# Kernel tuning notes

Measured on AMD Instinct MI355X. Metric: run time of the kernel, lower is better.

Reference implementation:

```python
import jax, jax.numpy as jnp
import numpy as np

B, D, H, O, S, K, T = 4096, 512, 1024, 512, 4, 4, 3


def setup_inputs() -> dict:
    key = jax.random.key(0)
    ks = iter(jax.random.split(key, 48))
    def w(*shape):
        return jax.random.normal(next(ks), shape, jnp.float32) * 0.02
    def z(*shape):
        return jnp.zeros(shape, jnp.float32)
    return {
        'user_emb': jax.random.normal(next(ks), (B, D), jnp.float32),
        # layer-1 shared experts (stacked over S): D -> H -> O
        's1_W1': w(S, D, H), 's1_b1': z(S, H), 's1_W2': w(S, H, O), 's1_b2': z(S, O),
        # layer-1 task experts (stacked over T tasks x K experts)
        't1_W1': w(T, K, D, H), 't1_b1': z(T, K, H), 't1_W2': w(T, K, H, O), 't1_b2': z(T, K, O),
        # layer-1 gates: T task gates (S+K outputs) + 1 combined gate (S+T*K outputs)
        'g1_W': w(T, D, S + K), 'g1_b': z(T, S + K),
        'g1l_W': w(D, S + T * K), 'g1l_b': z(S + T * K),
        # layer-2 shared / task experts: O -> H -> O
        's2_W1': w(S, O, H), 's2_b1': z(S, H), 's2_W2': w(S, H, O), 's2_b2': z(S, O),
        't2_W1': w(T, K, O, H), 't2_b1': z(T, K, H), 't2_W2': w(T, K, H, O), 't2_b2': z(T, K, O),
        'g2_W': w(T, O, S + K), 'g2_b': z(T, S + K),
        # churn tower: O -> 512 -> 256 -> 1
        'ch_W1': w(O, 512), 'ch_b1': z(512), 'ch_W2': w(512, 256), 'ch_b2': z(256), 'ch_W3': w(256, 1), 'ch_b3': z(1),
        # buy_sku + buy_cat towers stacked on leading axis 2: O -> 512 -> 256 -> 100
        'bt_W1': w(2, O, 512), 'bt_b1': z(2, 512), 'bt_W2': w(2, 512, 256), 'bt_b2': z(2, 256), 'bt_W3': w(2, 256, 100), 'bt_b3': z(2, 100),
    }


def _ple_forward(user_emb, s1_W1, s1_b1, s1_W2, s1_b2, t1_W1, t1_b1, t1_W2, t1_b2,
                 g1_W, g1_b, g1l_W, g1l_b, s2_W1, s2_b1, s2_W2, s2_b2,
                 t2_W1, t2_b1, t2_W2, t2_b2, g2_W, g2_b,
                 ch_W1, ch_b1, ch_W2, ch_b2, ch_W3, ch_b3,
                 bt_W1, bt_b1, bt_W2, bt_b2, bt_W3, bt_b3):
    relu = jax.nn.relu
    Bn = user_emb.shape[0]
    # ---- PLE layer 1 (dropout = identity in eval) ----
    sh1 = jnp.einsum('bsh,sho->bso', relu(jnp.einsum('bd,sdh->bsh', user_emb, s1_W1) + s1_b1), s1_W2) + s1_b2          # [B,S,O]
    tk1 = jnp.einsum('btkh,tkho->btko', relu(jnp.einsum('bd,tkdh->btkh', user_emb, t1_W1) + t1_b1), t1_W2) + t1_b2    # [B,T,K,O]
    g1 = jax.nn.softmax(jnp.einsum('bd,tde->tbe', user_emb, g1_W) + g1_b[:, None, :], axis=-1)                        # [T,B,S+K]
    g1l = jax.nn.softmax(user_emb @ g1l_W + g1l_b, axis=-1)                                                           # [B,S+T*K]
    # per-task concat: [shared, task_i] experts, gated combine (bmm)
    feats = jnp.concatenate([jnp.broadcast_to(sh1[:, None], (Bn, T, S, O)), tk1], axis=2)                             # [B,T,S+K,O]
    task_feats = jnp.einsum('tbe,bteo->tbo', g1, feats)                                                               # [T,B,O]
    # combined feat: order is [task_0..task_{T-1}, shared] per the torch code
    feats_last = jnp.concatenate([tk1.reshape(Bn, T * K, O), sh1], axis=1)                                            # [B,T*K+S,O]
    feat_last = jnp.einsum('be,beo->bo', g1l, feats_last)                                                             # [B,O]
    # ---- PLE layer 2 ----
    sh2 = jnp.einsum('bsh,sho->bso', relu(jnp.einsum('bo,soh->bsh', feat_last, s2_W1) + s2_b1), s2_W2) + s2_b2        # [B,S,O]
    tk2 = jnp.einsum('tbkh,tkho->tbko', relu(jnp.einsum('tbo,tkoh->tbkh', task_feats, t2_W1) + t2_b1[:, None]), t2_W2) + t2_b2[:, None]  # [T,B,K,O]
    g2 = jax.nn.softmax(jnp.einsum('tbo,toe->tbe', task_feats, g2_W) + g2_b[:, None, :], axis=-1)                     # [T,B,S+K]
    exp2 = jnp.concatenate([jnp.broadcast_to(sh2[None], (T, Bn, S, O)), tk2], axis=2)                                 # [T,B,S+K,O]
    tower_in = jnp.einsum('tbe,tbeo->tbo', g2, exp2)                                                                  # [T,B,O]
    # ---- towers ----
    churn = relu(relu(tower_in[0] @ ch_W1 + ch_b1) @ ch_W2 + ch_b2) @ ch_W3 + ch_b3                                   # [B,1]
    x = tower_in[1:3]                                                                                                 # [2,B,O]
    h = relu(jnp.einsum('nbo,noh->nbh', x, bt_W1) + bt_b1[:, None])
    h = relu(jnp.einsum('nbh,nhk->nbk', h, bt_W2) + bt_b2[:, None])
    out = jnp.einsum('nbk,nkm->nbm', h, bt_W3) + bt_b3[:, None]                                                       # [2,B,100]
    return churn, out[0], out[1]


def reference(user_emb, s1_W1, s1_b1, s1_W2, s1_b2, t1_W1, t1_b1, t1_W2, t1_b2,
              g1_W, g1_b, g1l_W, g1l_b, s2_W1, s2_b1, s2_W2, s2_b2,
              t2_W1, t2_b1, t2_W2, t2_b2, g2_W, g2_b,
              ch_W1, ch_b1, ch_W2, ch_b2, ch_W3, ch_b3,
              bt_W1, bt_b1, bt_W2, bt_b2, bt_W3, bt_b3):
    return _ple_forward(user_emb, s1_W1, s1_b1, s1_W2, s1_b2, t1_W1, t1_b1, t1_W2, t1_b2,
                        g1_W, g1_b, g1l_W, g1l_b, s2_W1, s2_b1, s2_W2, s2_b2,
                        t2_W1, t2_b1, t2_W2, t2_b2, g2_W, g2_b,
                        ch_W1, ch_b1, ch_W2, ch_b2, ch_W3, ch_b3,
                        bt_W1, bt_b1, bt_W2, bt_b2, bt_W3, bt_b3)
```

## Files before the change

kernel.cpp:

```cpp
#include <hip/hip_runtime.h>
#include <stdint.h>
#include <stddef.h>

typedef float f32x4 __attribute__((ext_vector_type(4)));
typedef int   i32x4 __attribute__((ext_vector_type(4)));
typedef _Float16 f16;
typedef _Float16 f16x8 __attribute__((ext_vector_type(8)));
typedef _Float16 f16x4 __attribute__((ext_vector_type(4)));

#define NB 4096

__device__ __forceinline__ size_t tiled_off(int m, int k, int K) {
  return (size_t)(m >> 7) * ((size_t)128 * K) + (size_t)(k >> 5) * 4096 +
         (size_t)(((k >> 3) & 3) * 1024 + (m & 127) * 8 + (k & 7));
}

__device__ __forceinline__ void gload_lds16(const f16* g, f16* l) {
  __builtin_amdgcn_global_load_lds(
      (const __attribute__((address_space(1))) void*)g,
      (__attribute__((address_space(3))) void*)l, 16, 0, 0);
}

struct GemmArgs {
  const f16* A[16];
  const f16* W[16];
  const float* bias[16];
  void* C[16];
  int N, K;
};

template<bool RELU, int OMODE>
__global__ __launch_bounds__(256, 4)
void gemm_kernel(GemmArgs args) {
  const int nwg = gridDim.x * gridDim.y * gridDim.z;
  int bid = blockIdx.x + gridDim.x * (blockIdx.y + gridDim.y * blockIdx.z);
  if ((nwg & 7) == 0) {
    const int cpx = nwg >> 3;
    bid = (bid & 7) * cpx + (bid >> 3);
  }
  const int gx  = bid % gridDim.x;
  const int rem = bid / gridDim.x;
  const int gy  = rem % gridDim.y;
  const int g   = rem / gridDim.y;
  const int n0 = gx * 128, m0 = gy * 128;

  const int tid = threadIdx.x;
  const int lane = tid & 63;
  const int wid = tid >> 6;
  const int wr = wid >> 1, wc = wid & 1;
  const int N = args.N, K = args.K;

  __shared__ __align__(16) f16 SH[16384];

  const f16* __restrict__ At = args.A[g] + (size_t)gy * 128 * K;
  const f16* __restrict__ Wt = args.W[g] + (size_t)gx * 128 * K;

  const int e0 = tid * 8, e1 = e0 + 2048;
  const int wb0 = (tid & ~63) * 8;
  const int wb1 = wb0 + 2048;

  f32x4 acc[4][4];
#pragma unroll
  for (int i = 0; i < 4; i++)
#pragma unroll
    for (int j = 0; j < 4; j++) { f32x4 z = {0.f, 0.f, 0.f, 0.f}; acc[i][j] = z; }

  const int nsteps = K >> 5;

  {
    f16* ab = SH;
    f16* bb = SH + 8192;
    gload_lds16(At + e0, ab + wb0);
    gload_lds16(At + e1, ab + wb1);
    gload_lds16(Wt + e0, bb + wb0);
    gload_lds16(Wt + e1, bb + wb1);
  }
  __syncthreads();

  for (int s = 0; s < nsteps; ++s) {
    const int cur = s & 1;
    if (s + 1 < nsteps) {
      const int nxt = cur ^ 1;
      const int off = (s + 1) << 12;
      f16* ab = SH + nxt * 4096;
      f16* bb = SH + 8192 + nxt * 4096;
      gload_lds16(At + off + e0, ab + wb0);
      gload_lds16(At + off + e1, ab + wb1);
      gload_lds16(Wt + off + e0, bb + wb0);
      gload_lds16(Wt + off + e1, bb + wb1);
    }
    const f16* ab = SH + cur * 4096;
    const f16* bb = SH + 8192 + cur * 4096;
    f16x8 af[4], bfv[4];
#pragma unroll
    for (int i = 0; i < 4; i++)
      af[i] = *(const f16x8*)(ab + (lane >> 4) * 1024 + (wr * 64 + i * 16 + (lane & 15)) * 8);
#pragma unroll
    for (int j = 0; j < 4; j++)
      bfv[j] = *(const f16x8*)(bb + (lane >> 4) * 1024 + (wc * 64 + j * 16 + (lane & 15)) * 8);
#pragma unroll
    for (int i = 0; i < 4; i++)
#pragma unroll
      for (int j = 0; j < 4; j++)
        acc[i][j] = __builtin_amdgcn_mfma_f32_16x16x32_f16(af[i], bfv[j], acc[i][j], 0, 0, 0);
    if (s + 1 < nsteps) __syncthreads();
  }

  const float* __restrict__ bias = args.bias[g];

  if constexpr (OMODE == 2) {
    __syncthreads();
#pragma unroll
    for (int j = 0; j < 4; j++) {
      const int col = wc * 64 + j * 16 + (lane & 15);
      const float bv = bias[n0 + col];
#pragma unroll
      for (int i = 0; i < 4; i++) {
        const int rowb = wr * 64 + i * 16 + ((lane >> 4) << 2);
#pragma unroll
        for (int q = 0; q < 4; q++) {
          float v = acc[i][j][q] + bv;
          if (RELU) v = fmaxf(v, 0.0f);
          SH[tiled_off(rowb + q, col, 128)] = (f16)v;
        }
      }
    }
    __syncthreads();
    f16* __restrict__ Cg = (f16*)args.C[g] + ((size_t)gy * N + n0) * 128;
#pragma unroll
    for (int r = 0; r < 8; r++) {
      const int c = r * 256 + tid;
      i32x4 v = *(const i32x4*)(SH + (size_t)c * 8);
      *(i32x4*)(Cg + (size_t)c * 8) = v;
    }
  } else {
#pragma unroll
    for (int j = 0; j < 4; j++) {
      const int n = n0 + wc * 64 + j * 16 + (lane & 15);
      if (n < N) {
        const float bv = bias[n];
#pragma unroll
        for (int i = 0; i < 4; i++) {
          const int mrow = m0 + wr * 64 + i * 16 + ((lane >> 4) << 2);
#pragma unroll
          for (int q = 0; q < 4; q++) {
            float v = acc[i][j][q] + bv;
            if (RELU) v = fmaxf(v, 0.0f);
            ((float*)args.C[g])[(size_t)(mrow + q) * N + n] = v;
          }
        }
      }
    }
  }
}

__global__ __launch_bounds__(256)
void transpose_cvt2_kernel(const float* __restrict__ srcA, int nA,
                           const float* __restrict__ srcB,
                           f16* __restrict__ dst, int K, int N, int dstStride) {
  __shared__ float tile[32][33];
  const int z = blockIdx.z;
  const float* __restrict__ src =
      (z < nA) ? srcA + (size_t)z * K * N : srcB + (size_t)(z - nA) * K * N;
  const size_t dof = (size_t)z * dstStride;
  const int kb = blockIdx.y * 32, nb = blockIdx.x * 32;
  const int tx = threadIdx.x, ty = threadIdx.y;
#pragma unroll
  for (int i = 0; i < 32; i += 8) {
    int k = kb + ty + i, n = nb + tx;
    tile[ty + i][tx] = (k < K && n < N) ? src[(size_t)k * N + n] : 0.f;
  }
  __syncthreads();
#pragma unroll
  for (int i = 0; i < 32; i += 8) {
    int n = nb + ty + i, k = kb + tx;
    if (n < N && k < K) dst[dof + tiled_off(n, k, K)] = (f16)tile[tx][ty + i];
  }
}

__global__ __launch_bounds__(256)
void cvt_kernel(const float* __restrict__ src, f16* __restrict__ dst, int n4) {
  int i = blockIdx.x * 256 + threadIdx.x;
  if (i < n4) {
    f32x4 v = *(const f32x4*)(src + (size_t)i * 4);
    f16x4 o = {(f16)v.x, (f16)v.y, (f16)v.z, (f16)v.w};
    const int e = i * 4;
    *(f16x4*)(dst + tiled_off(e >> 9, e & 511, 512)) = o;
  }
}

__global__ __launch_bounds__(256)
void gates1_kernel(const float* __restrict__ x, const float* __restrict__ g1W,
                   const float* __restrict__ g1b, const float* __restrict__ g1lW,
                   const float* __restrict__ g1lb, float* __restrict__ g1,
                   float* __restrict__ g1l) {
  const int lane = threadIdx.x & 63;
  const int b = blockIdx.x * 4 + (threadIdx.x >> 6);
  float xv[8];
#pragma unroll
  for (int i = 0; i < 8; i++) xv[i] = x[(size_t)b * 512 + lane + 64 * i];

#pragma unroll
  for (int t = 0; t < 3; t++) {
    float acc[8] = {0, 0, 0, 0, 0, 0, 0, 0};
#pragma unroll
    for (int i = 0; i < 8; i++) {
      const int d = lane + 64 * i;
      const float* wp = g1W + ((size_t)t * 512 + d) * 8;
      f32x4 w0 = *(const f32x4*)wp;
      f32x4 w1 = *(const f32x4*)(wp + 4);
      acc[0] += xv[i] * w0.x; acc[1] += xv[i] * w0.y;
      acc[2] += xv[i] * w0.z; acc[3] += xv[i] * w0.w;
      acc[4] += xv[i] * w1.x; acc[5] += xv[i] * w1.y;
      acc[6] += xv[i] * w1.z; acc[7] += xv[i] * w1.w;
    }
#pragma unroll
    for (int e = 0; e < 8; e++) {
#pragma unroll
      for (int off = 32; off >= 1; off >>= 1) acc[e] += __shfl_xor(acc[e], off);
      acc[e] += g1b[t * 8 + e];
    }
    float m = acc[0];
#pragma unroll
    for (int e = 1; e < 8; e++) m = fmaxf(m, acc[e]);
    float s = 0.f, p[8];
#pragma unroll
    for (int e = 0; e < 8; e++) { p[e] = expf(acc[e] - m); s += p[e]; }
    float inv = 1.0f / s;
    float mine = 0.f;
#pragma unroll
    for (int e = 0; e < 8; e++) if (lane == e) mine = p[e] * inv;
    if (lane < 8) g1[((size_t)t * NB + b) * 8 + lane] = mine;
  }

  float acc[16] = {};
#pragma unroll
  for (int i = 0; i < 8; i++) {
    const int d = lane + 64 * i;
    const float* wp = g1lW + (size_t)d * 16;
#pragma unroll
    for (int e4 = 0; e4 < 4; e4++) {
      f32x4 wv = *(const f32x4*)(wp + e4 * 4);
      acc[e4 * 4 + 0] += xv[i] * wv.x; acc[e4 * 4 + 1] += xv[i] * wv.y;
      acc[e4 * 4 + 2] += xv[i] * wv.z; acc[e4 * 4 + 3] += xv[i] * wv.w;
    }
  }
#pragma unroll
  for (int e = 0; e < 16; e++) {
#pragma unroll
    for (int off = 32; off >= 1; off >>= 1) acc[e] += __shfl_xor(acc[e], off);
    acc[e] += g1lb[e];
  }
  float m = acc[0];
#pragma unroll
  for (int e = 1; e < 16; e++) m = fmaxf(m, acc[e]);
  float s = 0.f, p[16];
#pragma unroll
  for (int e = 0; e < 16; e++) { p[e] = expf(acc[e] - m); s += p[e]; }
  float inv = 1.0f / s;
  float mine = 0.f;
#pragma unroll
  for (int e = 0; e < 16; e++) if (lane == e) mine = p[e] * inv;
  if (lane < 16) g1l[(size_t)b * 16 + lane] = mine;
}

__global__ __launch_bounds__(256)
void gates2_kernel(const f16* __restrict__ tf, const float* __restrict__ g2W,
                   const float* __restrict__ g2b, float* __restrict__ g2, int Bc) {
  const int lane = threadIdx.x & 63;
  const int b = blockIdx.x * 4 + (threadIdx.x >> 6);
  const int t = blockIdx.y;
  const f16* tb = tf + (size_t)t * Bc * 512;
  float xv[8];
#pragma unroll
  for (int i = 0; i < 8; i++)
    xv[i] = (float)tb[tiled_off(b, lane + 64 * i, 512)];
  float acc[8] = {0, 0, 0, 0, 0, 0, 0, 0};
#pragma unroll
  for (int i = 0; i < 8; i++) {
    const int d = lane + 64 * i;
    const float* wp = g2W + ((size_t)t * 512 + d) * 8;
    f32x4 w0 = *(const f32x4*)wp;
    f32x4 w1 = *(const f32x4*)(wp + 4);
    acc[0] += xv[i] * w0.x; acc[1] += xv[i] * w0.y;
    acc[2] += xv[i] * w0.z; acc[3] += xv[i] * w0.w;
    acc[4] += xv[i] * w1.x; acc[5] += xv[i] * w1.y;
    acc[6] += xv[i] * w1.z; acc[7] += xv[i] * w1.w;
  }
#pragma unroll
  for (int e = 0; e < 8; e++) {
#pragma unroll
    for (int off = 32; off >= 1; off >>= 1) acc[e] += __shfl_xor(acc[e], off);
    acc[e] += g2b[t * 8 + e];
  }
  float m = acc[0];
#pragma unroll
  for (int e = 1; e < 8; e++) m = fmaxf(m, acc[e]);
  float s = 0.f, p[8];
#pragma unroll
  for (int e = 0; e < 8; e++) { p[e] = expf(acc[e] - m); s += p[e]; }
  float inv = 1.0f / s;
  float mine = 0.f;
#pragma unroll
  for (int e = 0; e < 8; e++) if (lane == e) mine = p[e] * inv;
  if (lane < 8) g2[((size_t)t * Bc + b) * 8 + lane] = mine;
}

__global__ __launch_bounds__(256)
void combine1_kernel(const f16* __restrict__ E, const float* __restrict__ g1,
                     const float* __restrict__ g1l, f16* __restrict__ tfh,
                     f16* __restrict__ flh, int Bc) {
  const int t8 = blockIdx.x * 256 + threadIdx.x;
  const int b = ((t8 >> 13) << 7) | (t8 & 127);
  const size_t base = (size_t)t8 * 8;
  f16x8 ev[16];
#pragma unroll
  for (int i = 0; i < 16; i++)
    ev[i] = *(const f16x8*)(E + (size_t)i * Bc * 512 + base);
#pragma unroll
  for (int t = 0; t < 3; t++) {
    const float* g = g1 + ((size_t)t * NB + b) * 8;
    f16x8 o;
#pragma unroll
    for (int j = 0; j < 8; j++) {
      float v = g[0] * (float)ev[0][j] + g[1] * (float)ev[1][j] +
                g[2] * (float)ev[2][j] + g[3] * (float)ev[3][j];
#pragma unroll
      for (int k = 0; k < 4; k++) v += g[4 + k] * (float)ev[4 + 4 * t + k][j];
      o[j] = (f16)v;
    }
    *(f16x8*)(tfh + (size_t)t * Bc * 512 + base) = o;
  }
  const float* gl = g1l + (size_t)b * 16;
  f16x8 o;
#pragma unroll
  for (int j = 0; j < 8; j++) {
    float v = 0.f;
#pragma unroll
    for (int jj = 0; jj < 12; jj++) v += gl[jj] * (float)ev[4 + jj][j];
#pragma unroll
    for (int s2 = 0; s2 < 4; s2++) v += gl[12 + s2] * (float)ev[s2][j];
    o[j] = (f16)v;
  }
  *(f16x8*)(flh + base) = o;
}

__global__ __launch_bounds__(256)
void combine2_kernel(const f16* __restrict__ E2, const float* __restrict__ g2,
                     f16* __restrict__ tin, int Bc) {
  const int t = blockIdx.y;
  const int t8 = blockIdx.x * 256 + threadIdx.x;
  const int b = ((t8 >> 13) << 7) | (t8 & 127);
  const size_t base = (size_t)t8 * 8;
  const float* g = g2 + ((size_t)t * Bc + b) * 8;
  f16x8 es[8];
#pragma unroll
  for (int s2 = 0; s2 < 4; s2++)
    es[s2] = *(const f16x8*)(E2 + (size_t)s2 * Bc * 512 + base);
#pragma unroll
  for (int k = 0; k < 4; k++)
    es[4 + k] = *(const f16x8*)(E2 + (size_t)(4 + 4 * t + k) * Bc * 512 + base);
  f16x8 o;
#pragma unroll
  for (int j = 0; j < 8; j++) {
    float v = 0.f;
#pragma unroll
    for (int i = 0; i < 8; i++) v += g[i] * (float)es[i][j];
    o[j] = (f16)v;
  }
  *(f16x8*)(tin + (size_t)t * Bc * 512 + base) = o;
}

__global__ __launch_bounds__(256)
void churn_l3_kernel(const f16* __restrict__ TW2, const float* __restrict__ W3,
                     const float* __restrict__ b3, float* __restrict__ out) {
  const int lane = threadIdx.x & 63;
  const int b = blockIdx.x * 4 + (threadIdx.x >> 6);
  float s = 0.f;
#pragma unroll
  for (int i = 0; i < 4; i++) {
    int d = lane + 64 * i;
    s += (float)TW2[tiled_off(b, d, 256)] * W3[d];
  }
#pragma unroll
  for (int off = 32; off >= 1; off >>= 1) s += __shfl_xor(s, off);
  if (lane == 0) out[b] = s + b3[0];
}

extern "C" void kernel_launch(void* const* d_in, const int* in_sizes, int n_in,
                              void* d_out, int out_size, void* d_ws, size_t ws_size,
                              hipStream_t stream) {
  const float* user_emb = (const float*)d_in[0];
  const float* s1_W1 = (const float*)d_in[1];
  const float* s1_b1 = (const float*)d_in[2];
  const float* s1_W2 = (const float*)d_in[3];
  const float* s1_b2 = (const float*)d_in[4];
  const float* t1_W1 = (const float*)d_in[5];
  const float* t1_b1 = (const float*)d_in[6];
  const float* t1_W2 = (const float*)d_in[7];
  const float* t1_b2 = (const float*)d_in[8];
  const float* g1_W  = (const float*)d_in[9];
  const float* g1_b  = (const float*)d_in[10];
  const float* g1l_W = (const float*)d_in[11];
  const float* g1l_b = (const float*)d_in[12];
  const float* s2_W1 = (const float*)d_in[13];
  const float* s2_b1 = (const float*)d_in[14];
  const float* s2_W2 = (const float*)d_in[15];
  const float* s2_b2 = (const float*)d_in[16];
  const float* t2_W1 = (const float*)d_in[17];
  const float* t2_b1 = (const float*)d_in[18];
  const float* t2_W2 = (const float*)d_in[19];
  const float* t2_b2 = (const float*)d_in[20];
  const float* g2_W  = (const float*)d_in[21];
  const float* g2_b  = (const float*)d_in[22];
  const float* ch_W1 = (const float*)d_in[23];
  const float* ch_b1 = (const float*)d_in[24];
  const float* ch_W2 = (const float*)d_in[25];
  const float* ch_b2 = (const float*)d_in[26];
  const float* ch_W3 = (const float*)d_in[27];
  const float* ch_b3 = (const float*)d_in[28];
  const float* bt_W1 = (const float*)d_in[29];
  const float* bt_b1 = (const float*)d_in[30];
  const float* bt_W2 = (const float*)d_in[31];
  const float* bt_b2 = (const float*)d_in[32];
  const float* bt_W3 = (const float*)d_in[33];
  const float* bt_b3 = (const float*)d_in[34];

  const size_t PERSIST = 74800000ull;
  const size_t PERCHUNK_PER_ROW = 61024ull;
  int Bc = 4096;
  while (Bc > 256 &&
         PERSIST + PERCHUNK_PER_ROW * (size_t)Bc + (64ull << 10) > ws_size)
    Bc >>= 1;
  const int nchunks = NB / Bc;

  char* w = (char*)d_ws;
  auto alloc = [&](size_t bytes) {
    char* p = w;
    w += (bytes + 255) & ~(size_t)255;
    return p;
  };
  f16* WT1 = (f16*)alloc(16ull * 512 * 1024 * 2);
  f16* WT2 = (f16*)alloc(16ull * 1024 * 512 * 2);
  f16* WT3 = (f16*)alloc(16ull * 512 * 1024 * 2);
  f16* WT4 = (f16*)alloc(16ull * 1024 * 512 * 2);
  f16* WT5 = (f16*)alloc(3ull * 512 * 512 * 2);
  f16* WT6 = (f16*)alloc(3ull * 256 * 512 * 2);
  f16* WT7 = (f16*)alloc(2ull * 128 * 256 * 2);
  f16* Uemb = (f16*)alloc((size_t)NB * 512 * 2);
  float* B1  = (float*)alloc(16384 * 4);
  float* B2  = (float*)alloc(8192 * 4);
  float* B3  = (float*)alloc(16384 * 4);
  float* B4  = (float*)alloc(8192 * 4);
  float* BT1 = (float*)alloc(1536 * 4);
  float* BT2 = (float*)alloc(768 * 4);
  float* G1  = (float*)alloc(3ull * NB * 8 * 4);
  float* G1L = (float*)alloc((size_t)NB * 16 * 4);
  f16*   Hc   = (f16*)alloc(16ull * Bc * 1024 * 2);
  f16*   Ec   = (f16*)alloc(16ull * Bc * 512 * 2);
  f16*   TFh  = (f16*)alloc(3ull * Bc * 512 * 2);
  f16*   FLh  = (f16*)alloc((size_t)Bc * 512 * 2);
  float* G2c  = (float*)alloc(3ull * Bc * 8 * 4);
  f16*   TINc = (f16*)alloc(3ull * Bc * 512 * 2);
  f16*   TW1c = (f16*)alloc(3ull * Bc * 512 * 2);
  f16*   TW2c = (f16*)alloc(3ull * Bc * 256 * 2);
  if ((size_t)(w - (char*)d_ws) > ws_size) return;

  hipMemcpyAsync(B1, s1_b1, 4 * 1024 * 4, hipMemcpyDeviceToDevice, stream);
  hipMemcpyAsync(B1 + 4096, t1_b1, 12 * 1024 * 4, hipMemcpyDeviceToDevice, stream);
  hipMemcpyAsync(B2, s1_b2, 4 * 512 * 4, hipMemcpyDeviceToDevice, stream);
  hipMemcpyAsync(B2 + 2048, t1_b2, 12 * 512 * 4, hipMemcpyDeviceToDevice, stream);
  hipMemcpyAsync(B3, s2_b1, 4 * 1024 * 4, hipMemcpyDeviceToDevice, stream);
  hipMemcpyAsync(B3 + 4096, t2_b1, 12 * 1024 * 4, hipMemcpyDeviceToDevice, stream);
  hipMemcpyAsync(B4, s2_b2, 4 * 512 * 4, hipMemcpyDeviceToDevice, stream);
  hipMemcpyAsync(B4 + 2048, t2_b2, 12 * 512 * 4, hipMemcpyDeviceToDevice, stream);
  hipMemcpyAsync(BT1, ch_b1, 512 * 4, hipMemcpyDeviceToDevice, stream);
  hipMemcpyAsync(BT1 + 512, bt_b1, 2 * 512 * 4, hipMemcpyDeviceToDevice, stream);
  hipMemcpyAsync(BT2, ch_b2, 256 * 4, hipMemcpyDeviceToDevice, stream);
  hipMemcpyAsync(BT2 + 256, bt_b2, 2 * 256 * 4, hipMemcpyDeviceToDevice, stream);
  hipMemsetAsync(WT7, 0, 2ull * 128 * 256 * 2, stream);

  dim3 tb(32, 8);
  transpose_cvt2_kernel<<<dim3(32, 16, 16), tb, 0, stream>>>(s1_W1, 4, t1_W1, WT1, 512, 1024, 512 * 1024);
  transpose_cvt2_kernel<<<dim3(16, 32, 16), tb, 0, stream>>>(s1_W2, 4, t1_W2, WT2, 1024, 512, 1024 * 512);
  transpose_cvt2_kernel<<<dim3(32, 16, 16), tb, 0, stream>>>(s2_W1, 4, t2_W1, WT3, 512, 1024, 512 * 1024);
  transpose_cvt2_kernel<<<dim3(16, 32, 16), tb, 0, stream>>>(s2_W2, 4, t2_W2, WT4, 1024, 512, 1024 * 512);
  transpose_cvt2_kernel<<<dim3(16, 16, 3), tb, 0, stream>>>(ch_W1, 1, bt_W1, WT5, 512, 512, 512 * 512);
  transpose_cvt2_kernel<<<dim3(8, 16, 3), tb, 0, stream>>>(ch_W2, 1, bt_W2, WT6, 512, 256, 256 * 512);
  transpose_cvt2_kernel<<<dim3(4, 8, 2), tb, 0, stream>>>(bt_W3, 2, nullptr, WT7, 256, 100, 128 * 256);
  cvt_kernel<<<2048, 256, 0, stream>>>(user_emb, Uemb, NB * 512 / 4);
  gates1_kernel<<<NB / 4, 256, 0, stream>>>(user_emb, g1_W, g1_b, g1l_W, g1l_b, G1, G1L);

  GemmArgs ga;
  const int MB = Bc / 128;

  for (int c = 0; c < nchunks; ++c) {
    const int b0 = c * Bc;

    ga.N = 1024; ga.K = 512;
    for (int g = 0; g < 16; g++) {
      ga.A[g] = Uemb + (size_t)b0 * 512;
      ga.W[g] = WT1 + (size_t)g * 512 * 1024;
      ga.bias[g] = B1 + g * 1024;
      ga.C[g] = Hc + (size_t)g * Bc * 1024;
    }
    gemm_kernel<true, 2><<<dim3(8, MB, 16), 256, 0, stream>>>(ga);

    ga.N = 512; ga.K = 1024;
    for (int g = 0; g < 16; g++) {
      ga.A[g] = Hc + (size_t)g * Bc * 1024;
      ga.W[g] = WT2 + (size_t)g * 1024 * 512;
      ga.bias[g] = B2 + g * 512;
      ga.C[g] = Ec + (size_t)g * Bc * 512;
    }
    gemm_kernel<false, 2><<<dim3(4, MB, 16), 256, 0, stream>>>(ga);

    combine1_kernel<<<Bc / 4, 256, 0, stream>>>(
        Ec, G1 + (size_t)b0 * 8, G1L + (size_t)b0 * 16, TFh, FLh, Bc);
    gates2_kernel<<<dim3(Bc / 4, 3), 256, 0, stream>>>(TFh, g2_W, g2_b, G2c, Bc);

    ga.N = 1024; ga.K = 512;
    for (int g = 0; g < 16; g++) {
      ga.A[g] = (g < 4) ? FLh : TFh + (size_t)((g - 4) >> 2) * Bc * 512;
      ga.W[g] = WT3 + (size_t)g * 512 * 1024;
      ga.bias[g] = B3 + g * 1024;
      ga.C[g] = Hc + (size_t)g * Bc * 1024;
    }
    gemm_kernel<true, 2><<<dim3(8, MB, 16), 256, 0, stream>>>(ga);

    ga.N = 512; ga.K = 1024;
    for (int g = 0; g < 16; g++) {
      ga.A[g] = Hc + (size_t)g * Bc * 1024;
      ga.W[g] = WT4 + (size_t)g * 1024 * 512;
      ga.bias[g] = B4 + g * 512;
      ga.C[g] = Ec + (size_t)g * Bc * 512;
    }
    gemm_kernel<false, 2><<<dim3(4, MB, 16), 256, 0, stream>>>(ga);

    combine2_kernel<<<dim3(Bc / 4, 3), 256, 0, stream>>>(Ec, G2c, TINc, Bc);

    ga.N = 512; ga.K = 512;
    for (int g = 0; g < 3; g++) {
      ga.A[g] = TINc + (size_t)g * Bc * 512;
      ga.W[g] = WT5 + (size_t)g * 512 * 512;
      ga.bias[g] = BT1 + g * 512;
      ga.C[g] = TW1c + (size_t)g * Bc * 512;
    }
    for (int g = 3; g < 16; g++) { ga.A[g] = ga.A[0]; ga.W[g] = ga.W[0]; ga.bias[g] = ga.bias[0]; ga.C[g] = ga.C[0]; }
    gemm_kernel<true, 2><<<dim3(4, MB, 3), 256, 0, stream>>>(ga);

    ga.N = 256; ga.K = 512;
    for (int g = 0; g < 3; g++) {
      ga.A[g] = TW1c + (size_t)g * Bc * 512;
      ga.W[g] = WT6 + (size_t)g * 256 * 512;
      ga.bias[g] = BT2 + g * 256;
      ga.C[g] = TW2c + (size_t)g * Bc * 256;
    }
    for (int g = 3; g < 16; g++) { ga.A[g] = ga.A[0]; ga.W[g] = ga.W[0]; ga.bias[g] = ga.bias[0]; ga.C[g] = ga.C[0]; }
    gemm_kernel<true, 2><<<dim3(2, MB, 3), 256, 0, stream>>>(ga);

    churn_l3_kernel<<<Bc / 4, 256, 0, stream>>>(TW2c, ch_W3, ch_b3,
                                                (float*)d_out + b0);

    ga.N = 100; ga.K = 256;
    for (int g = 0; g < 2; g++) {
      ga.A[g] = TW2c + (size_t)(1 + g) * Bc * 256;
      ga.W[g] = WT7 + (size_t)g * 128 * 256;
      ga.bias[g] = bt_b3 + g * 100;
      ga.C[g] = (float*)d_out + NB + (size_t)g * NB * 100 + (size_t)b0 * 100;
    }
    for (int g = 2; g < 16; g++) { ga.A[g] = ga.A[0]; ga.W[g] = ga.W[0]; ga.bias[g] = ga.bias[0]; ga.C[g] = ga.C[0]; }
    gemm_kernel<false, 0><<<dim3(1, MB, 2), 256, 0, stream>>>(ga);
  }
}
```

Baseline: 545.9 us.

## Vectorize weight transpose, fuse bias packing into one kernel, swizzle GEMM epilogue LDS

Rewrites the weight transpose/convert kernel to use 64x64 tiles with float4 global loads and 16-byte f16x8 stores. Replaces twelve device-to-device bias memcpys and a memset with a single packing kernel, cutting per-call launch overhead. Adds an XOR swizzle to the GEMM f16 epilogue's shared-memory staging to reduce bank conflicts. The transpose relies on K being a multiple of 64 and uses a larger shared tile, which may lower occupancy.

Result: faster. 504.4 us (-7.6%).

```diff
diff --git a/kernel.cpp b/kernel.cpp
--- a/kernel.cpp
+++ b/kernel.cpp
@@ -110,6 +110,7 @@
 
   if constexpr (OMODE == 2) {
     __syncthreads();
+    const int swz = (((lane >> 3) & 1) << 3) | (((lane >> 5) & 1) << 4);
 #pragma unroll
     for (int j = 0; j < 4; j++) {
       const int col = wc * 64 + j * 16 + (lane & 15);
@@ -121,7 +122,7 @@
         for (int q = 0; q < 4; q++) {
           float v = acc[i][j][q] + bv;
           if (RELU) v = fmaxf(v, 0.0f);
-          SH[tiled_off(rowb + q, col, 128)] = (f16)v;
+          SH[tiled_off(rowb + q, col, 128) ^ swz] = (f16)v;
         }
       }
     }
@@ -130,7 +131,8 @@
 #pragma unroll
     for (int r = 0; r < 8; r++) {
       const int c = r * 256 + tid;
-      i32x4 v = *(const i32x4*)(SH + (size_t)c * 8);
+      const int te = (c * 8) ^ (((c >> 7) & 1) << 3) ^ (((c >> 3) & 1) << 4);
+      i32x4 v = *(const i32x4*)(SH + te);
       *(i32x4*)(Cg + (size_t)c * 8) = v;
     }
   } else {
@@ -158,23 +160,42 @@
 void transpose_cvt2_kernel(const float* __restrict__ srcA, int nA,
                            const float* __restrict__ srcB,
                            f16* __restrict__ dst, int K, int N, int dstStride) {
-  __shared__ float tile[32][33];
+  __shared__ float tile[64][67];
   const int z = blockIdx.z;
   const float* __restrict__ src =
       (z < nA) ? srcA + (size_t)z * K * N : srcB + (size_t)(z - nA) * K * N;
   const size_t dof = (size_t)z * dstStride;
-  const int kb = blockIdx.y * 32, nb = blockIdx.x * 32;
-  const int tx = threadIdx.x, ty = threadIdx.y;
-#pragma unroll
-  for (int i = 0; i < 32; i += 8) {
-    int k = kb + ty + i, n = nb + tx;
-    tile[ty + i][tx] = (k < K && n < N) ? src[(size_t)k * N + n] : 0.f;
+  const int nb = blockIdx.x * 64, kb = blockIdx.y * 64;
+  const int tid = threadIdx.x;
+  const int krow = tid >> 4;
+  const int n4 = (tid & 15) * 4;
+#pragma unroll
+  for (int i = 0; i < 4; i++) {
+    const int kk = krow + i * 16;
+    const int k = kb + kk;
+    const int n = nb + n4;
+    if (n + 3 < N) {
+      f32x4 v = *(const f32x4*)(src + (size_t)k * N + n);
+      tile[kk][n4 + 0] = v.x; tile[kk][n4 + 1] = v.y;
+      tile[kk][n4 + 2] = v.z; tile[kk][n4 + 3] = v.w;
+    } else {
+#pragma unroll
+      for (int e = 0; e < 4; e++)
+        tile[kk][n4 + e] = (n + e < N) ? src[(size_t)k * N + n + e] : 0.f;
+    }
   }
   __syncthreads();
-#pragma unroll
-  for (int i = 0; i < 32; i += 8) {
-    int n = nb + ty + i, k = kb + tx;
-    if (n < N && k < K) dst[dof + tiled_off(n, k, K)] = (f16)tile[tx][ty + i];
+  const int o = tid >> 5;
+  const int nl = tid & 31;
+#pragma unroll
+  for (int j = 0; j < 2; j++) {
+    const int n = nl + j * 32;
+    if (nb + n < N) {
+      f16x8 v;
+#pragma unroll
+      for (int e = 0; e < 8; e++) v[e] = (f16)tile[o * 8 + e][n];
+      *(f16x8*)(dst + dof + tiled_off(nb + n, kb + o * 8, K)) = v;
+    }
   }
 }
 
@@ -187,6 +208,30 @@
     const int e = i * 4;
     *(f16x4*)(dst + tiled_off(e >> 9, e & 511, 512)) = o;
   }
+}
+
+__global__ __launch_bounds__(256)
+void pack_kernel(float* B1, const float* s1b1, const float* t1b1,
+                 float* B2, const float* s1b2, const float* t1b2,
+                 float* B3, const float* s2b1, const float* t2b1,
+                 float* B4, const float* s2b2, const float* t2b2,
+                 float* BT1, const float* chb1, const float* btb1,
+                 float* BT2, const float* chb2, const float* btb2,
+                 uint32_t* wt7z) {
+  int i = blockIdx.x * 256 + threadIdx.x;
+  if (i < 16384) { B1[i] = (i < 4096) ? s1b1[i] : t1b1[i - 4096]; return; }
+  i -= 16384;
+  if (i < 8192)  { B2[i] = (i < 2048) ? s1b2[i] : t1b2[i - 2048]; return; }
+  i -= 8192;
+  if (i < 16384) { B3[i] = (i < 4096) ? s2b1[i] : t2b1[i - 4096]; return; }
+  i -= 16384;
+  if (i < 8192)  { B4[i] = (i < 2048) ? s2b2[i] : t2b2[i - 2048]; return; }
+  i -= 8192;
+  if (i < 1536)  { BT1[i] = (i < 512) ? chb1[i] : btb1[i - 512]; return; }
+  i -= 1536;
+  if (i < 768)   { BT2[i] = (i < 256) ? chb2[i] : btb2[i - 256]; return; }
+  i -= 768;
+  if (i < 32768) wt7z[i] = 0u;
 }
 
 __global__ __launch_bounds__(256)
@@ -466,28 +511,18 @@
   f16*   TW2c = (f16*)alloc(3ull * Bc * 256 * 2);
   if ((size_t)(w - (char*)d_ws) > ws_size) return;
 
-  hipMemcpyAsync(B1, s1_b1, 4 * 1024 * 4, hipMemcpyDeviceToDevice, stream);
-  hipMemcpyAsync(B1 + 4096, t1_b1, 12 * 1024 * 4, hipMemcpyDeviceToDevice, stream);
-  hipMemcpyAsync(B2, s1_b2, 4 * 512 * 4, hipMemcpyDeviceToDevice, stream);
-  hipMemcpyAsync(B2 + 2048, t1_b2, 12 * 512 * 4, hipMemcpyDeviceToDevice, stream);
-  hipMemcpyAsync(B3, s2_b1, 4 * 1024 * 4, hipMemcpyDeviceToDevice, stream);
-  hipMemcpyAsync(B3 + 4096, t2_b1, 12 * 1024 * 4, hipMemcpyDeviceToDevice, stream);
-  hipMemcpyAsync(B4, s2_b2, 4 * 512 * 4, hipMemcpyDeviceToDevice, stream);
-  hipMemcpyAsync(B4 + 2048, t2_b2, 12 * 512 * 4, hipMemcpyDeviceToDevice, stream);
-  hipMemcpyAsync(BT1, ch_b1, 512 * 4, hipMemcpyDeviceToDevice, stream);
-  hipMemcpyAsync(BT1 + 512, bt_b1, 2 * 512 * 4, hipMemcpyDeviceToDevice, stream);
-  hipMemcpyAsync(BT2, ch_b2, 256 * 4, hipMemcpyDeviceToDevice, stream);
-  hipMemcpyAsync(BT2 + 256, bt_b2, 2 * 256 * 4, hipMemcpyDeviceToDevice, stream);
-  hipMemsetAsync(WT7, 0, 2ull * 128 * 256 * 2, stream);
-
-  dim3 tb(32, 8);
-  transpose_cvt2_kernel<<<dim3(32, 16, 16), tb, 0, stream>>>(s1_W1, 4, t1_W1, WT1, 512, 1024, 512 * 1024);
-  transpose_cvt2_kernel<<<dim3(16, 32, 16), tb, 0, stream>>>(s1_W2, 4, t1_W2, WT2, 1024, 512, 1024 * 512);
-  transpose_cvt2_kernel<<<dim3(32, 16, 16), tb, 0, stream>>>(s2_W1, 4, t2_W1, WT3, 512, 1024, 512 * 1024);
-  transpose_cvt2_kernel<<<dim3(16, 32, 16), tb, 0, stream>>>(s2_W2, 4, t2_W2, WT4, 1024, 512, 1024 * 512);
-  transpose_cvt2_kernel<<<dim3(16, 16, 3), tb, 0, stream>>>(ch_W1, 1, bt_W1, WT5, 512, 512, 512 * 512);
-  transpose_cvt2_kernel<<<dim3(8, 16, 3), tb, 0, stream>>>(ch_W2, 1, bt_W2, WT6, 512, 256, 256 * 512);
-  transpose_cvt2_kernel<<<dim3(4, 8, 2), tb, 0, stream>>>(bt_W3, 2, nullptr, WT7, 256, 100, 128 * 256);
+  pack_kernel<<<329, 256, 0, stream>>>(B1, s1_b1, t1_b1, B2, s1_b2, t1_b2,
+                                       B3, s2_b1, t2_b1, B4, s2_b2, t2_b2,
+                                       BT1, ch_b1, bt_b1, BT2, ch_b2, bt_b2,
+                                       (uint32_t*)WT7);
+
+  transpose_cvt2_kernel<<<dim3(16, 8, 16), 256, 0, stream>>>(s1_W1, 4, t1_W1, WT1, 512, 1024, 512 * 1024);
+  transpose_cvt2_kernel<<<dim3(8, 16, 16), 256, 0, stream>>>(s1_W2, 4, t1_W2, WT2, 1024, 512, 1024 * 512);
+  transpose_cvt2_kernel<<<dim3(16, 8, 16), 256, 0, stream>>>(s2_W1, 4, t2_W1, WT3, 512, 1024, 512 * 1024);
+  transpose_cvt2_kernel<<<dim3(8, 16, 16), 256, 0, stream>>>(s2_W2, 4, t2_W2, WT4, 1024, 512, 1024 * 512);
+  transpose_cvt2_kernel<<<dim3(8, 8, 3), 256, 0, stream>>>(ch_W1, 1, bt_W1, WT5, 512, 512, 512 * 512);
+  transpose_cvt2_kernel<<<dim3(4, 8, 3), 256, 0, stream>>>(ch_W2, 1, bt_W2, WT6, 512, 256, 256 * 512);
+  transpose_cvt2_kernel<<<dim3(2, 4, 2), 256, 0, stream>>>(bt_W3, 2, nullptr, WT7, 256, 100, 128 * 256);
   cvt_kernel<<<2048, 256, 0, stream>>>(user_emb, Uemb, NB * 512 / 4);
   gates1_kernel<<<NB / 4, 256, 0, stream>>>(user_emb, g1_W, g1_b, g1l_W, g1l_b, G1, G1L);
 
```
